# Kernel optimization log

Measured on AMD Instinct MI355X. Metric: run time of the kernel, lower is better.

Reference implementation:

```python
import jax, jax.numpy as jnp
import numpy as np
from jax import lax

TOPK = 2


def setup_inputs() -> dict:
    key = jax.random.key(0)
    k1, k2, k3, k4 = jax.random.split(key, 4)
    B, T, D, E = 4, 2048, 1024, 8
    x = jax.random.normal(k1, (B, T, D), dtype=jnp.float32)
    gate_w = jax.random.normal(k2, (E, D), dtype=jnp.float32) * 0.02
    w_fc = jax.random.normal(k3, (E, 4 * D, D), dtype=jnp.float32) * 0.02
    w_proj = jax.random.normal(k4, (E, D, 4 * D), dtype=jnp.float32) * 0.02
    return {"x": x, "gate_w": gate_w, "w_fc": w_fc, "w_proj": w_proj}


def reference(x, gate_w, w_fc, w_proj):
    B, T, D = x.shape
    E = gate_w.shape[0]
    N = B * T
    xf = x.reshape(N, D)

    # gating
    gate_logits = xf @ gate_w.T                      # [N, E]
    gate_probs = jax.nn.softmax(gate_logits, axis=-1)
    routing_weights, expert_indices = lax.top_k(gate_probs, TOPK)  # [N, K]
    routing_weights = routing_weights / routing_weights.sum(axis=-1, keepdims=True)

    # combine weights per (token, expert); top-k indices are distinct per token
    hot = jax.nn.one_hot(expert_indices, E, dtype=xf.dtype)        # [N, K, E]
    comb = jnp.einsum('nke,nk->ne', hot, routing_weights)          # [N, E]
    tok_sel = hot.sum(axis=1)                                      # [N, E] in {0,1}
    expert_freq = tok_sel.mean(axis=0)                             # [E]

    # per-expert MLP (relu^2), accumulated over experts via scan
    def step(acc, xs):
        w1, w2, ce = xs                      # [4D,D], [D,4D], [N]
        h = jnp.square(jax.nn.relu(xf @ w1.T))   # [N, 4D]
        y = h @ w2.T                             # [N, D]
        return acc + ce[:, None] * y, None

    out, _ = lax.scan(step, jnp.zeros_like(xf), (w_fc, w_proj, comb.T))
    out = out.reshape(B, T, D)

    balance_loss = (gate_probs.mean(axis=0) * lax.stop_gradient(expert_freq)).sum() * E
    return out, balance_loss
```

## Files before the change

### kernel.cpp

```cpp
#include <hip/hip_runtime.h>
#include <hip/hip_bf16.h>

#define NTOK 8192
#define DDIM 1024
#define HDIM 4096
#define NEXP 8
#define NPAIR (NTOK * 2)
#define NMTILE 136
#define NPADROW (NPAIR + NEXP * 128)

typedef __attribute__((ext_vector_type(8))) short short8;
typedef __attribute__((ext_vector_type(4))) float floatx4;

__device__ __forceinline__ unsigned short f2bf(float f) {
  unsigned u = __float_as_uint(f);
  u += 0x7fffu + ((u >> 16) & 1u);
  return (unsigned short)(u >> 16);
}

__device__ __forceinline__ void async_copy16(const void* g, void* l) {
  __builtin_amdgcn_global_load_lds(
      (const __attribute__((address_space(1))) unsigned int*)g,
      (__attribute__((address_space(3))) unsigned int*)l, 16, 0, 0);
}

__global__ void cast_kernel(const float* __restrict__ src,
                            unsigned short* __restrict__ dst, int n4) {
  int i = blockIdx.x * 256 + threadIdx.x;
  if (i >= n4) return;
  const float4 v = ((const float4*)src)[i];
  ushort4 o;
  o.x = f2bf(v.x); o.y = f2bf(v.y); o.z = f2bf(v.z); o.w = f2bf(v.w);
  ((ushort4*)dst)[i] = o;
}

__global__ __launch_bounds__(256) void gating_kernel(
    const float* __restrict__ x, const float* __restrict__ gw,
    int* __restrict__ selE, float* __restrict__ selW,
    int* __restrict__ cnt, float* __restrict__ psum) {
  __shared__ float gws[NEXP * DDIM];
  __shared__ float pblk[4][NEXP];
  __shared__ int cblk[NEXP];
  const int t = threadIdx.x;
  for (int i = t; i < NEXP * DDIM; i += 256) gws[i] = gw[i];
  if (t < NEXP) cblk[t] = 0;
  __syncthreads();
  const int wv = t >> 6, lane = t & 63;
  const int tok = blockIdx.x * 4 + wv;
  double acc[NEXP];
#pragma unroll
  for (int e = 0; e < NEXP; e++) acc[e] = 0.0;
  const float* xr = x + (size_t)tok * DDIM;
  for (int i = lane; i < DDIM; i += 64) {
    double xv = (double)xr[i];
#pragma unroll
    for (int e = 0; e < NEXP; e++) acc[e] += xv * (double)gws[e * DDIM + i];
  }
#pragma unroll
  for (int e = 0; e < NEXP; e++)
    for (int off = 32; off > 0; off >>= 1) acc[e] += __shfl_xor(acc[e], off, 64);
  if (lane == 0) {
    double mx = acc[0];
    for (int e = 1; e < NEXP; e++) mx = acc[e] > mx ? acc[e] : mx;
    double p[NEXP], s = 0.0;
    for (int e = 0; e < NEXP; e++) { p[e] = exp(acc[e] - mx); s += p[e]; }
    int e1 = 0; double b1 = p[0];
    for (int e = 1; e < NEXP; e++) if (p[e] > b1) { b1 = p[e]; e1 = e; }
    int e2 = -1; double b2 = -1.0;
    for (int e = 0; e < NEXP; e++) if (e != e1 && p[e] > b2) { b2 = p[e]; e2 = e; }
    double rs = b1 + b2;
    selE[tok * 2 + 0] = e1; selE[tok * 2 + 1] = e2;
    selW[tok * 2 + 0] = (float)(b1 / rs); selW[tok * 2 + 1] = (float)(b2 / rs);
    atomicAdd(&cblk[e1], 1); atomicAdd(&cblk[e2], 1);
    for (int e = 0; e < NEXP; e++) pblk[wv][e] = (float)(p[e] / s);
  }
  __syncthreads();
  if (t < NEXP) {
    float sp = pblk[0][t] + pblk[1][t] + pblk[2][t] + pblk[3][t];
    atomicAdd(&psum[t], sp);
    if (cblk[t]) atomicAdd(&cnt[t], cblk[t]);
  }
}

__global__ void finalize_kernel(const int* __restrict__ cnt,
                                const float* __restrict__ psum,
                                int* __restrict__ abase, int* __restrict__ fill,
                                int* __restrict__ tile2exp,
                                float* __restrict__ loss_out) {
  for (int t = 0; t < NMTILE; t++) tile2exp[t] = -1;
  int b = 0;
  for (int e = 0; e < NEXP; e++) {
    abase[e] = b;
    fill[e] = b;
    int nt = (cnt[e] + 127) >> 7;
    for (int j = 0; j < nt; j++) tile2exp[(b >> 7) + j] = e;
    b += nt << 7;
  }
  abase[NEXP] = b;
  double L = 0.0;
  for (int e = 0; e < NEXP; e++) L += (double)psum[e] * (double)cnt[e];
  *loss_out = (float)(L * (double)NEXP / ((double)NTOK * (double)NTOK));
}

__global__ void scatter_kernel(const int* __restrict__ selE,
                               const float* __restrict__ selW,
                               int* __restrict__ fill, int* __restrict__ pairtok,
                               float* __restrict__ pairw, int* __restrict__ invmap) {
  int n = blockIdx.x * 256 + threadIdx.x;
  if (n >= NTOK) return;
  for (int k = 0; k < 2; k++) {
    int e = selE[n * 2 + k];
    int pos = atomicAdd(&fill[e], 1);
    pairtok[pos] = n;
    pairw[pos] = selW[n * 2 + k];
    invmap[n * 2 + k] = pos;
  }
}

__global__ __launch_bounds__(256) void combine_kernel(
    const float* __restrict__ ybuf, const int* __restrict__ invmap,
    float* __restrict__ out) {
  const int tok = blockIdx.x;
  const int c = threadIdx.x;
  const int p1 = invmap[tok * 2 + 0];
  const int p2 = invmap[tok * 2 + 1];
  const float4 a = ((const float4*)(ybuf + (size_t)p1 * DDIM))[c];
  const float4 b = ((const float4*)(ybuf + (size_t)p2 * DDIM))[c];
  float4 o;
  o.x = a.x + b.x; o.y = a.y + b.y; o.z = a.z + b.z; o.w = a.w + b.w;
  ((float4*)(out + (size_t)tok * DDIM))[c] = o;
}

template <int KD, int ND, int MODE>
__global__ __launch_bounds__(256) void moe_gemm(
    const unsigned short* __restrict__ A, const unsigned short* __restrict__ B,
    const int* __restrict__ abase, const int* __restrict__ cnt,
    const int* __restrict__ tile2exp, const int* __restrict__ pairtok,
    const float* __restrict__ pairw, unsigned short* __restrict__ hbuf,
    float* __restrict__ ybuf) {
  constexpr int NT = ND / 128;
  constexpr int KT = KD / 32;

  const int nwg = NT * NMTILE;
  const int lid = blockIdx.y * NT + blockIdx.x;
  const int q8 = nwg >> 3, r8 = nwg & 7;
  const int xcd = lid & 7, sub = lid >> 3;
  const int cbase = (xcd < r8) ? xcd * (q8 + 1) : r8 * (q8 + 1) + (xcd - r8) * q8;
  const int nlid = cbase + sub;
  const int mtile = nlid / NT;
  const int ntile = nlid - mtile * NT;

  const int e = tile2exp[mtile];
  if (e < 0) return;
  const int m0 = abase[e];
  const int cntE = cnt[e];
  const int mloc = mtile * 128 - m0;

  __shared__ unsigned short ldsA[2][4096];
  __shared__ unsigned short ldsB[2][4096];

  const int t = threadIdx.x, w = t >> 6, lane = t & 63;

  const unsigned short* gA[2];
  const unsigned short* gB[2];
  int soff[2];
#pragma unroll
  for (int i = 0; i < 2; i++) {
    const int c = w * 128 + i * 64 + lane;
    const int row = c >> 2;
    const int q = (c & 3) ^ (row & 3) ^ ((row >> 2) & 3);
    soff[i] = (w * 128 + i * 64) * 8;
    int ar = mloc + row;
    if (ar > cntE - 1) ar = cntE - 1;
    size_t arow;
    if (MODE == 0) arow = (size_t)pairtok[m0 + ar];
    else           arow = (size_t)(m0 + ar);
    gA[i] = A + arow * (size_t)KD + q * 8;
    gB[i] = B + ((size_t)e * ND + (ntile * 128 + row)) * (size_t)KD + q * 8;
  }

  const int wm = (w & 1) * 64, wn = (w >> 1) * 64;
  const int sw = (lane >> 4) ^ (lane & 3) ^ ((lane >> 2) & 3);
  int aoff[4], boff[4];
#pragma unroll
  for (int i = 0; i < 4; i++) {
    aoff[i] = (wm + i * 16 + (lane & 15)) * 4 + sw;
    boff[i] = (wn + i * 16 + (lane & 15)) * 4 + sw;
  }

  floatx4 acc[4][4] = {};

#pragma unroll
  for (int i = 0; i < 2; i++) {
    async_copy16(gA[i], &ldsA[0][soff[i]]);
    async_copy16(gB[i], &ldsB[0][soff[i]]);
  }
  __syncthreads();

#pragma unroll 2
  for (int kt = 0; kt < KT; kt++) {
    const int cur = kt & 1;
    if (kt + 1 < KT) {
#pragma unroll
      for (int i = 0; i < 2; i++) {
        async_copy16(gA[i] + (kt + 1) * 32, &ldsA[cur ^ 1][soff[i]]);
        async_copy16(gB[i] + (kt + 1) * 32, &ldsB[cur ^ 1][soff[i]]);
      }
    }
    short8 a[4], b[4];
#pragma unroll
    for (int i = 0; i < 4; i++) {
      a[i] = ((const short8*)ldsA[cur])[aoff[i]];
      b[i] = ((const short8*)ldsB[cur])[boff[i]];
    }
#pragma unroll
    for (int im = 0; im < 4; im++)
#pragma unroll
      for (int in = 0; in < 4; in++)
        acc[im][in] = __builtin_amdgcn_mfma_f32_16x16x32_bf16(a[im], b[in], acc[im][in], 0, 0, 0);
    __syncthreads();
  }

  const int Mv = cntE - mloc;
#pragma unroll
  for (int im = 0; im < 4; im++) {
#pragma unroll
    for (int r = 0; r < 4; r++) {
      const int rl = wm + im * 16 + (lane >> 4) * 4 + r;
      if (rl < Mv) {
        const int pr = m0 + mloc + rl;
        if (MODE == 0) {
#pragma unroll
          for (int in = 0; in < 4; in++) {
            float v = acc[im][in][r];
            v = v > 0.f ? v * v : 0.f;
            const int col = ntile * 128 + wn + in * 16 + (lane & 15);
            hbuf[(size_t)pr * HDIM + col] = f2bf(v);
          }
        } else {
          const float wgt = pairw[pr];
          float* yrow = ybuf + (size_t)pr * DDIM;
#pragma unroll
          for (int in = 0; in < 4; in++) {
            const int col = ntile * 128 + wn + in * 16 + (lane & 15);
            yrow[col] = wgt * acc[im][in][r];
          }
        }
      }
    }
  }
}

extern "C" void kernel_launch(void* const* d_in, const int* in_sizes, int n_in,
                              void* d_out, int out_size, void* d_ws, size_t ws_size,
                              hipStream_t stream) {
  const float* x   = (const float*)d_in[0];
  const float* gw  = (const float*)d_in[1];
  const float* wfc = (const float*)d_in[2];
  const float* wpj = (const float*)d_in[3];
  float* out = (float*)d_out;

  char* ws = (char*)d_ws;
  size_t off = 0;
  auto alloc = [&](size_t bytes) -> void* {
    void* p = ws + off;
    off += (bytes + 255) & ~(size_t)255;
    return p;
  };
  unsigned short* xb   = (unsigned short*)alloc((size_t)NTOK * DDIM * 2);
  unsigned short* wfcb = (unsigned short*)alloc((size_t)NEXP * HDIM * DDIM * 2);
  unsigned short* wpjb = (unsigned short*)alloc((size_t)NEXP * DDIM * HDIM * 2);
  unsigned short* hbuf = (unsigned short*)alloc((size_t)NPADROW * HDIM * 2);
  float* ybuf          = (float*)alloc((size_t)NPADROW * DDIM * 4);
  int*   pairtok = (int*)alloc(NPADROW * 4);
  float* pairw   = (float*)alloc(NPADROW * 4);
  int*   invmap  = (int*)alloc(NPAIR * 4);
  int*   selE    = (int*)alloc(NTOK * 2 * 4);
  float* selW    = (float*)alloc(NTOK * 2 * 4);
  int*   ctr     = (int*)alloc(1024);
  int* cnt = ctr; int* fill = ctr + 8; int* abase = ctr + 16;
  float* psum = (float*)(ctr + 28);
  int* tile2exp = ctr + 40;

  hipMemsetAsync(ctr, 0, 1024, stream);

  cast_kernel<<<(NTOK * DDIM / 4 + 255) / 256, 256, 0, stream>>>(x, xb, NTOK * DDIM / 4);
  cast_kernel<<<(NEXP * HDIM * DDIM / 4 + 255) / 256, 256, 0, stream>>>(wfc, wfcb, NEXP * HDIM * DDIM / 4);
  cast_kernel<<<(NEXP * DDIM * HDIM / 4 + 255) / 256, 256, 0, stream>>>(wpj, wpjb, NEXP * DDIM * HDIM / 4);

  gating_kernel<<<NTOK / 4, 256, 0, stream>>>(x, gw, selE, selW, cnt, psum);
  finalize_kernel<<<1, 1, 0, stream>>>(cnt, psum, abase, fill, tile2exp,
                                       out + (size_t)NTOK * DDIM);
  scatter_kernel<<<NTOK / 256, 256, 0, stream>>>(selE, selW, fill, pairtok, pairw, invmap);

  moe_gemm<DDIM, HDIM, 0><<<dim3(HDIM / 128, NMTILE), 256, 0, stream>>>(
      xb, wfcb, abase, cnt, tile2exp, pairtok, pairw, hbuf, nullptr);
  moe_gemm<HDIM, DDIM, 1><<<dim3(DDIM / 128, NMTILE), 256, 0, stream>>>(
      hbuf, wpjb, abase, cnt, tile2exp, pairtok, pairw, nullptr, ybuf);

  combine_kernel<<<NTOK, 256, 0, stream>>>(ybuf, invmap, out);
}
```

Measured before the change: 889.3 us.

## Widen MoE GEMM tiles, deepen async pipeline, fuse combine via atomics

The grouped GEMM moves from 128x128 tiles on 256 threads to 128x256 tiles on 512 threads, with a 4-stage LDS ring holding two tiles in flight, explicit waitcnt/barrier scheduling and priority bumps around the MFMA block. The second GEMM now atomically adds weighted results straight into the output, which removes the fp32 ybuf round trip and the combine kernel. The output has to be memset first. Finalize becomes a 256-thread kernel, and scatter uses block-local histograms to cut global atomic contention. Float atomics make the summation order nondeterministic, and the larger tiles reduce the number of workgroups.

New measurement: 978.1 us. 10.0% more time.

```diff
diff --git a/kernel.cpp b/kernel.cpp
--- a/kernel.cpp
+++ b/kernel.cpp
@@ -82,63 +82,70 @@
   }
 }
 
-__global__ void finalize_kernel(const int* __restrict__ cnt,
-                                const float* __restrict__ psum,
-                                int* __restrict__ abase, int* __restrict__ fill,
-                                int* __restrict__ tile2exp,
-                                float* __restrict__ loss_out) {
-  for (int t = 0; t < NMTILE; t++) tile2exp[t] = -1;
-  int b = 0;
-  for (int e = 0; e < NEXP; e++) {
-    abase[e] = b;
-    fill[e] = b;
-    int nt = (cnt[e] + 127) >> 7;
-    for (int j = 0; j < nt; j++) tile2exp[(b >> 7) + j] = e;
-    b += nt << 7;
-  }
-  abase[NEXP] = b;
-  double L = 0.0;
-  for (int e = 0; e < NEXP; e++) L += (double)psum[e] * (double)cnt[e];
-  *loss_out = (float)(L * (double)NEXP / ((double)NTOK * (double)NTOK));
-}
-
-__global__ void scatter_kernel(const int* __restrict__ selE,
-                               const float* __restrict__ selW,
-                               int* __restrict__ fill, int* __restrict__ pairtok,
-                               float* __restrict__ pairw, int* __restrict__ invmap) {
-  int n = blockIdx.x * 256 + threadIdx.x;
-  if (n >= NTOK) return;
-  for (int k = 0; k < 2; k++) {
-    int e = selE[n * 2 + k];
-    int pos = atomicAdd(&fill[e], 1);
-    pairtok[pos] = n;
-    pairw[pos] = selW[n * 2 + k];
-    invmap[n * 2 + k] = pos;
-  }
-}
-
-__global__ __launch_bounds__(256) void combine_kernel(
-    const float* __restrict__ ybuf, const int* __restrict__ invmap,
-    float* __restrict__ out) {
-  const int tok = blockIdx.x;
-  const int c = threadIdx.x;
-  const int p1 = invmap[tok * 2 + 0];
-  const int p2 = invmap[tok * 2 + 1];
-  const float4 a = ((const float4*)(ybuf + (size_t)p1 * DDIM))[c];
-  const float4 b = ((const float4*)(ybuf + (size_t)p2 * DDIM))[c];
-  float4 o;
-  o.x = a.x + b.x; o.y = a.y + b.y; o.z = a.z + b.z; o.w = a.w + b.w;
-  ((float4*)(out + (size_t)tok * DDIM))[c] = o;
+__global__ __launch_bounds__(256) void finalize_kernel(
+    const int* __restrict__ cnt, const float* __restrict__ psum,
+    int* __restrict__ abase, int* __restrict__ fill,
+    int* __restrict__ tile2exp, float* __restrict__ loss_out) {
+  __shared__ int sb[NEXP + 1];
+  __shared__ int scnt[NEXP];
+  const int t = threadIdx.x;
+  if (t == 0) {
+    int b = 0;
+    for (int e = 0; e < NEXP; e++) {
+      int c = cnt[e];
+      scnt[e] = c; sb[e] = b;
+      b += ((c + 127) >> 7) << 7;
+    }
+    sb[NEXP] = b;
+  }
+  __syncthreads();
+  if (t < NEXP) { abase[t] = sb[t]; fill[t] = sb[t]; }
+  if (t == NEXP) abase[NEXP] = sb[NEXP];
+  for (int i = t; i < NMTILE; i += 256) {
+    int ex = -1;
+#pragma unroll
+    for (int e = 0; e < NEXP; e++) {
+      int t0 = sb[e] >> 7, nt = (scnt[e] + 127) >> 7;
+      if (i >= t0 && i < t0 + nt) ex = e;
+    }
+    tile2exp[i] = ex;
+  }
+  if (t == 0) {
+    double L = 0.0;
+    for (int e = 0; e < NEXP; e++) L += (double)psum[e] * (double)scnt[e];
+    *loss_out = (float)(L * (double)NEXP / ((double)NTOK * (double)NTOK));
+  }
+}
+
+__global__ __launch_bounds__(256) void scatter_kernel(
+    const int* __restrict__ selE, const float* __restrict__ selW,
+    int* __restrict__ fill, int* __restrict__ pairtok, float* __restrict__ pairw) {
+  __shared__ int h1[NEXP], h2[NEXP], base[NEXP];
+  const int t = threadIdx.x;
+  if (t < NEXP) { h1[t] = 0; h2[t] = 0; }
+  __syncthreads();
+  const int n = blockIdx.x * 256 + t;
+  const int e0 = selE[n * 2 + 0], e1 = selE[n * 2 + 1];
+  atomicAdd(&h1[e0], 1); atomicAdd(&h1[e1], 1);
+  __syncthreads();
+  if (t < NEXP && h1[t]) base[t] = atomicAdd(&fill[t], h1[t]);
+  __syncthreads();
+  int r0 = atomicAdd(&h2[e0], 1);
+  int p0 = base[e0] + r0;
+  pairtok[p0] = n; pairw[p0] = selW[n * 2 + 0];
+  int r1 = atomicAdd(&h2[e1], 1);
+  int p1 = base[e1] + r1;
+  pairtok[p1] = n; pairw[p1] = selW[n * 2 + 1];
 }
 
 template <int KD, int ND, int MODE>
-__global__ __launch_bounds__(256) void moe_gemm(
+__global__ __launch_bounds__(512, 1) void moe_gemm(
     const unsigned short* __restrict__ A, const unsigned short* __restrict__ B,
     const int* __restrict__ abase, const int* __restrict__ cnt,
     const int* __restrict__ tile2exp, const int* __restrict__ pairtok,
     const float* __restrict__ pairw, unsigned short* __restrict__ hbuf,
-    float* __restrict__ ybuf) {
-  constexpr int NT = ND / 128;
+    float* __restrict__ out) {
+  constexpr int NT = ND / 256;
   constexpr int KT = KD / 32;
 
   const int nwg = NT * NMTILE;
@@ -156,69 +163,79 @@
   const int cntE = cnt[e];
   const int mloc = mtile * 128 - m0;
 
-  __shared__ unsigned short ldsA[2][4096];
-  __shared__ unsigned short ldsB[2][4096];
+  __shared__ unsigned short ldsA[4][512 * 8];
+  __shared__ unsigned short ldsB[4][1024 * 8];
 
   const int t = threadIdx.x, w = t >> 6, lane = t & 63;
 
-  const unsigned short* gA[2];
+  const int cA = t;
+  const int rowA = cA >> 2;
+  const int qA = (cA & 3) ^ (rowA & 3) ^ ((rowA >> 2) & 3);
+  int ar = mloc + rowA;
+  if (ar > cntE - 1) ar = cntE - 1;
+  size_t arow;
+  if (MODE == 0) arow = (size_t)pairtok[m0 + ar];
+  else           arow = (size_t)(m0 + ar);
+  const unsigned short* gA = A + arow * (size_t)KD + qA * 8;
+  const int dstAoff = (w * 64) * 8;
+
   const unsigned short* gB[2];
-  int soff[2];
+  int dstBoff[2];
 #pragma unroll
   for (int i = 0; i < 2; i++) {
-    const int c = w * 128 + i * 64 + lane;
-    const int row = c >> 2;
-    const int q = (c & 3) ^ (row & 3) ^ ((row >> 2) & 3);
-    soff[i] = (w * 128 + i * 64) * 8;
-    int ar = mloc + row;
-    if (ar > cntE - 1) ar = cntE - 1;
-    size_t arow;
-    if (MODE == 0) arow = (size_t)pairtok[m0 + ar];
-    else           arow = (size_t)(m0 + ar);
-    gA[i] = A + arow * (size_t)KD + q * 8;
-    gB[i] = B + ((size_t)e * ND + (ntile * 128 + row)) * (size_t)KD + q * 8;
-  }
-
-  const int wm = (w & 1) * 64, wn = (w >> 1) * 64;
+    const int p = i * 512 + t;
+    const int rowB = p >> 2;
+    const int qB = (p & 3) ^ (rowB & 3) ^ ((rowB >> 2) & 3);
+    gB[i] = B + ((size_t)e * ND + (ntile * 256 + rowB)) * (size_t)KD + qB * 8;
+    dstBoff[i] = (i * 512 + w * 64) * 8;
+  }
+
+  const int wr = w >> 2, wc = w & 3;
   const int sw = (lane >> 4) ^ (lane & 3) ^ ((lane >> 2) & 3);
-  int aoff[4], boff[4];
+  int apos[4], bpos[4];
 #pragma unroll
   for (int i = 0; i < 4; i++) {
-    aoff[i] = (wm + i * 16 + (lane & 15)) * 4 + sw;
-    boff[i] = (wn + i * 16 + (lane & 15)) * 4 + sw;
+    apos[i] = (wr * 64 + i * 16 + (lane & 15)) * 4 + sw;
+    bpos[i] = (wc * 64 + i * 16 + (lane & 15)) * 4 + sw;
   }
 
   floatx4 acc[4][4] = {};
 
-#pragma unroll
-  for (int i = 0; i < 2; i++) {
-    async_copy16(gA[i], &ldsA[0][soff[i]]);
-    async_copy16(gB[i], &ldsB[0][soff[i]]);
-  }
-  __syncthreads();
-
-#pragma unroll 2
-  for (int kt = 0; kt < KT; kt++) {
-    const int cur = kt & 1;
-    if (kt + 1 < KT) {
-#pragma unroll
-      for (int i = 0; i < 2; i++) {
-        async_copy16(gA[i] + (kt + 1) * 32, &ldsA[cur ^ 1][soff[i]]);
-        async_copy16(gB[i] + (kt + 1) * 32, &ldsB[cur ^ 1][soff[i]]);
-      }
+  auto stage = [&](int kt2) {
+    const int s = kt2 & 3;
+    const int ko = kt2 * 32;
+    async_copy16(gA + ko, &ldsA[s][dstAoff]);
+    async_copy16(gB[0] + ko, &ldsB[s][dstBoff[0]]);
+    async_copy16(gB[1] + ko, &ldsB[s][dstBoff[1]]);
+  };
+
+  stage(0);
+  stage(1);
+  asm volatile("s_waitcnt vmcnt(3)" ::: "memory");
+  __builtin_amdgcn_s_barrier();
+
+#pragma unroll 4
+  for (int kt = 0; kt < KT; ++kt) {
+    const int s = kt & 3;
+    short8 a[4], b[4];
+#pragma unroll
+    for (int i = 0; i < 4; i++) {
+      a[i] = ((const short8*)ldsA[s])[apos[i]];
+      b[i] = ((const short8*)ldsB[s])[bpos[i]];
     }
-    short8 a[4], b[4];
-#pragma unroll
-    for (int i = 0; i < 4; i++) {
-      a[i] = ((const short8*)ldsA[cur])[aoff[i]];
-      b[i] = ((const short8*)ldsB[cur])[boff[i]];
-    }
+    if (kt + 2 < KT) stage(kt + 2);
+    __builtin_amdgcn_s_barrier();
+    asm volatile("s_waitcnt lgkmcnt(0)" ::: "memory");
+    __builtin_amdgcn_s_setprio(1);
 #pragma unroll
     for (int im = 0; im < 4; im++)
 #pragma unroll
       for (int in = 0; in < 4; in++)
         acc[im][in] = __builtin_amdgcn_mfma_f32_16x16x32_bf16(a[im], b[in], acc[im][in], 0, 0, 0);
-    __syncthreads();
+    __builtin_amdgcn_s_setprio(0);
+    if (kt + 2 < KT) asm volatile("s_waitcnt vmcnt(3)" ::: "memory");
+    else             asm volatile("s_waitcnt vmcnt(0)" ::: "memory");
+    __builtin_amdgcn_s_barrier();
   }
 
   const int Mv = cntE - mloc;
@@ -226,7 +243,7 @@
   for (int im = 0; im < 4; im++) {
 #pragma unroll
     for (int r = 0; r < 4; r++) {
-      const int rl = wm + im * 16 + (lane >> 4) * 4 + r;
+      const int rl = wr * 64 + im * 16 + (lane >> 4) * 4 + r;
       if (rl < Mv) {
         const int pr = m0 + mloc + rl;
         if (MODE == 0) {
@@ -234,16 +251,17 @@
           for (int in = 0; in < 4; in++) {
             float v = acc[im][in][r];
             v = v > 0.f ? v * v : 0.f;
-            const int col = ntile * 128 + wn + in * 16 + (lane & 15);
+            const int col = ntile * 256 + wc * 64 + in * 16 + (lane & 15);
             hbuf[(size_t)pr * HDIM + col] = f2bf(v);
           }
         } else {
           const float wgt = pairw[pr];
-          float* yrow = ybuf + (size_t)pr * DDIM;
+          const int tok = pairtok[pr];
+          float* yrow = out + (size_t)tok * DDIM;
 #pragma unroll
           for (int in = 0; in < 4; in++) {
-            const int col = ntile * 128 + wn + in * 16 + (lane & 15);
-            yrow[col] = wgt * acc[im][in][r];
+            const int col = ntile * 256 + wc * 64 + in * 16 + (lane & 15);
+            atomicAdd(yrow + col, wgt * acc[im][in][r]);
           }
         }
       }
@@ -271,10 +289,8 @@
   unsigned short* wfcb = (unsigned short*)alloc((size_t)NEXP * HDIM * DDIM * 2);
   unsigned short* wpjb = (unsigned short*)alloc((size_t)NEXP * DDIM * HDIM * 2);
   unsigned short* hbuf = (unsigned short*)alloc((size_t)NPADROW * HDIM * 2);
-  float* ybuf          = (float*)alloc((size_t)NPADROW * DDIM * 4);
   int*   pairtok = (int*)alloc(NPADROW * 4);
   float* pairw   = (float*)alloc(NPADROW * 4);
-  int*   invmap  = (int*)alloc(NPAIR * 4);
   int*   selE    = (int*)alloc(NTOK * 2 * 4);
   float* selW    = (float*)alloc(NTOK * 2 * 4);
   int*   ctr     = (int*)alloc(1024);
@@ -283,20 +299,19 @@
   int* tile2exp = ctr + 40;
 
   hipMemsetAsync(ctr, 0, 1024, stream);
+  hipMemsetAsync(out, 0, (size_t)NTOK * DDIM * 4, stream);
 
   cast_kernel<<<(NTOK * DDIM / 4 + 255) / 256, 256, 0, stream>>>(x, xb, NTOK * DDIM / 4);
   cast_kernel<<<(NEXP * HDIM * DDIM / 4 + 255) / 256, 256, 0, stream>>>(wfc, wfcb, NEXP * HDIM * DDIM / 4);
   cast_kernel<<<(NEXP * DDIM * HDIM / 4 + 255) / 256, 256, 0, stream>>>(wpj, wpjb, NEXP * DDIM * HDIM / 4);
 
   gating_kernel<<<NTOK / 4, 256, 0, stream>>>(x, gw, selE, selW, cnt, psum);
-  finalize_kernel<<<1, 1, 0, stream>>>(cnt, psum, abase, fill, tile2exp,
-                                       out + (size_t)NTOK * DDIM);
-  scatter_kernel<<<NTOK / 256, 256, 0, stream>>>(selE, selW, fill, pairtok, pairw, invmap);
-
-  moe_gemm<DDIM, HDIM, 0><<<dim3(HDIM / 128, NMTILE), 256, 0, stream>>>(
+  finalize_kernel<<<1, 256, 0, stream>>>(cnt, psum, abase, fill, tile2exp,
+                                         out + (size_t)NTOK * DDIM);
+  scatter_kernel<<<NTOK / 256, 256, 0, stream>>>(selE, selW, fill, pairtok, pairw);
+
+  moe_gemm<DDIM, HDIM, 0><<<dim3(HDIM / 256, NMTILE), 512, 0, stream>>>(
       xb, wfcb, abase, cnt, tile2exp, pairtok, pairw, hbuf, nullptr);
-  moe_gemm<HDIM, DDIM, 1><<<dim3(DDIM / 128, NMTILE), 256, 0, stream>>>(
-      hbuf, wpjb, abase, cnt, tile2exp, pairtok, pairw, nullptr, ybuf);
-
-  combine_kernel<<<NTOK, 256, 0, stream>>>(ybuf, invmap, out);
-}
+  moe_gemm<HDIM, DDIM, 1><<<dim3(DDIM / 256, NMTILE), 512, 0, stream>>>(
+      hbuf, wpjb, abase, cnt, tile2exp, pairtok, pairw, nullptr, out);
+}
```
